# Kernel tuning notes

Measured on AMD Instinct MI355X. Metric: run time of the kernel, lower is better.

The kernel has to match this reference:

```python
import jax, jax.numpy as jnp
import numpy as np

N, V = 256, 5
D_DX, D_RX = 48, 48
C = 128            # code_dim
DEMO_F, DEMO_D = 32, 64
DT, NH, DFF = 256, 8, 2048
REP, HID = 128, 256
NE, NC = 2, 64
VOC_DX = (1000, 5000, 20000)
VOC_RX = (100, 500, 2000, 5000)
NEG = -1e20

def _ln(x, s, b):
    m = jnp.mean(x, -1, keepdims=True)
    v = jnp.var(x, -1, keepdims=True)
    return (x - m) / jnp.sqrt(v + 1e-5) * s + b

def _pe(seq, d):
    pos = jnp.arange(seq, dtype=jnp.float32)[:, None]
    i = jnp.arange(0, d, 2, dtype=jnp.float32)
    ang = pos / jnp.power(10000.0, i / d)
    pe = jnp.zeros((seq, d), jnp.float32)
    pe = pe.at[:, 0::2].set(jnp.sin(ang))
    pe = pe.at[:, 1::2].set(jnp.cos(ang))
    return pe

def _mha(x, qw, qb, ow_, ob_):
    n, s, d = x.shape
    hd = d // NH
    q, k, v = jnp.split(x @ qw + qb, 3, axis=-1)
    q = q.reshape(n, s, NH, hd); k = k.reshape(n, s, NH, hd); v = v.reshape(n, s, NH, hd)
    att = jax.nn.softmax(jnp.einsum('bqhd,bkhd->bhqk', q, k) / jnp.sqrt(jnp.float32(hd)), axis=-1)
    return jnp.einsum('bhqk,bkhd->bqhd', att, v).reshape(n, s, d) @ ow_ + ob_

def _enc_layer(x, qw, qb, ow_, ob_, l1s, l1b, f1w, f1b, f2w, f2b, l2s, l2b):
    x = _ln(x + _mha(x, qw, qb, ow_, ob_), l1s, l1b)            # post-norm, as nn.TransformerEncoderLayer default
    ff = jnp.maximum(x @ f1w + f1b, 0.0) @ f2w + f2b
    return _ln(x + ff, l2s, l2b)

def setup_inputs() -> dict:
    key = jax.random.key(0)
    ks = iter(jax.random.split(key, 96))
    def nrm(shape, scale=0.02):
        return jax.random.normal(next(ks), shape, jnp.float32) * scale
    def zeros(shape): return jnp.zeros(shape, jnp.float32)
    def ones(shape): return jnp.ones(shape, jnp.float32)
    inp = {}
    inp['x_dx_l1'] = jax.random.randint(next(ks), (N, V, D_DX), 0, VOC_DX[0])
    inp['x_dx_l2'] = jax.random.randint(next(ks), (N, V, D_DX), 0, VOC_DX[1])
    inp['x_dx_l3'] = jax.random.randint(next(ks), (N, V, D_DX), 0, VOC_DX[2])
    inp['x_rx_l1'] = jax.random.randint(next(ks), (N, V, D_RX), 0, VOC_RX[0])
    inp['x_rx_l2'] = jax.random.randint(next(ks), (N, V, D_RX), 0, VOC_RX[1])
    inp['x_rx_l3'] = jax.random.randint(next(ks), (N, V, D_RX), 0, VOC_RX[2])
    inp['x_rx_l4'] = jax.random.randint(next(ks), (N, V, D_RX), 0, VOC_RX[3])
    inp['x_demo'] = jax.random.normal(next(ks), (N, V, DEMO_F), jnp.float32)
    inp['W_demo'] = nrm((DEMO_F, DEMO_D)); inp['b_demo'] = zeros((DEMO_D,))
    inp['E_dx1'] = nrm((VOC_DX[0], C)); inp['E_dx2'] = nrm((VOC_DX[1], C)); inp['E_dx3'] = nrm((VOC_DX[2], C))
    inp['E_rx1'] = nrm((VOC_RX[0], C)); inp['E_rx2'] = nrm((VOC_RX[1], C))
    inp['E_rx3'] = nrm((VOC_RX[2], C)); inp['E_rx4'] = nrm((VOC_RX[3], C))
    inp['We_dx'] = nrm((2 * C, 1)); inp['be_dx'] = zeros((1,))
    inp['We_rx'] = nrm((2 * C, 1)); inp['be_rx'] = zeros((1,))
    inp['Wev_dx'] = nrm((C, 1)); inp['bev_dx'] = zeros((1,))
    inp['Wev_rx'] = nrm((C, 1)); inp['bev_rx'] = zeros((1,))
    inp['Wcv'] = nrm((REP, 1)); inp['bcv'] = zeros((1,))
    inp['enc_w1'] = nrm((DEMO_D + C, DT)); inp['enc_b1'] = zeros((DT,))
    inp['qkv_w'] = nrm((4, DT, 3 * DT)); inp['qkv_b'] = zeros((4, 3 * DT))
    inp['ow'] = nrm((4, DT, DT)); inp['ob'] = zeros((4, DT))
    inp['ln1s'] = ones((4, DT)); inp['ln1b'] = zeros((4, DT))
    inp['ff1w'] = nrm((4, DT, DFF)); inp['ff1b'] = zeros((4, DFF))
    inp['ff2w'] = nrm((4, DFF, DT)); inp['ff2b'] = zeros((4, DT))
    inp['ln2s'] = ones((4, DT)); inp['ln2b'] = zeros((4, DT))
    inp['enc_w2'] = nrm((DT, REP)); inp['enc_b2'] = zeros((REP,))
    inp['mlp_w'] = nrm((REP, REP // 2)); inp['mlp_b'] = zeros((REP // 2,))
    inp['mlp2_w'] = nrm((REP // 2, REP // 2)); inp['mlp2_b'] = zeros((REP // 2,))
    inp['fc1w'] = nrm((NE, REP, HID)); inp['fc1b'] = zeros((NE, HID))
    inp['fc2w'] = nrm((NE, HID, HID // 2)); inp['fc2b'] = zeros((NE, HID // 2))
    inp['fc3w'] = nrm((NE, HID // 2, NC)); inp['fc3b'] = zeros((NE, NC))
    return inp

def reference(x_dx_l1, x_dx_l2, x_dx_l3, x_rx_l1, x_rx_l2, x_rx_l3, x_rx_l4, x_demo,
              W_demo, b_demo, E_dx1, E_dx2, E_dx3, E_rx1, E_rx2, E_rx3, E_rx4,
              We_dx, be_dx, We_rx, be_rx, Wev_dx, bev_dx, Wev_rx, bev_rx, Wcv, bcv,
              enc_w1, enc_b1, qkv_w, qkv_b, ow, ob, ln1s, ln1b, ff1w, ff1b, ff2w, ff2b,
              ln2s, ln2b, enc_w2, enc_b2, mlp_w, mlp_b, mlp2_w, mlp2_b,
              fc1w, fc1b, fc2w, fc2b, fc3w, fc3b):
    # ---- GRAM context vectors (dropout is identity at inference) ----
    emb_dx = jnp.stack([E_dx1[x_dx_l1], E_dx2[x_dx_l2], E_dx3[x_dx_l3]], axis=-2)          # [N,V,D,3,C]
    cat_dx = jnp.concatenate([jnp.broadcast_to(emb_dx[..., 2:3, :], emb_dx.shape), emb_dx], axis=-1)
    en_dx = jnp.maximum(cat_dx @ We_dx + be_dx, 0.0)                                       # [N,V,D,3,1]
    en_dx = jnp.where((x_dx_l1 != 0)[..., None, None], en_dx, NEG)
    att_dx = jax.nn.softmax(en_dx, axis=-2)
    cv_dx = jnp.einsum('nvdr,nvdrc->nvdc', att_dx[..., 0], emb_dx)                          # [N,V,D,C]

    emb_rx = jnp.stack([E_rx1[x_rx_l1], E_rx2[x_rx_l2], E_rx3[x_rx_l3], E_rx4[x_rx_l4]], axis=-2)  # [N,V,D,4,C]
    cat_rx = jnp.concatenate([jnp.broadcast_to(emb_rx[..., 3:4, :], emb_rx.shape), emb_rx], axis=-1)
    en_rx = jnp.maximum(cat_rx @ We_rx + be_rx, 0.0)
    en_rx = jnp.where((x_rx_l1 != 0)[..., None, None], en_rx, NEG)
    att_rx = jax.nn.softmax(en_rx, axis=-2)
    cv_rx = jnp.einsum('nvdr,nvdrc->nvdc', att_rx[..., 0], emb_rx)

    # ---- visit-level attention pooling over concatenated codes ----
    context = jnp.concatenate([cv_dx, cv_rx], axis=-2)                                      # [N,V,Ddx+Drx,C]
    ev_dx = jnp.where((x_dx_l1 != 0)[..., None], cv_dx @ Wev_dx + bev_dx, NEG)
    ev_rx = jnp.where((x_rx_l1 != 0)[..., None], cv_rx @ Wev_rx + bev_rx, NEG)
    att_v = jax.nn.softmax(jnp.concatenate([ev_dx, ev_rx], axis=-2), axis=-2)               # [N,V,M,1]
    ccv = jnp.einsum('nvm,nvmc->nvc', att_v[..., 0], context)                               # [N,V,C]

    # ---- shared transformer encoder ----
    demo = jnp.maximum(x_demo @ W_demo + b_demo, 0.0)
    x = jnp.concatenate([demo, ccv], axis=-1) @ enc_w1 + enc_b1
    x = x + _pe(V, DT)[None]
    for i in range(4):
        x = _enc_layer(x, qkv_w[i], qkv_b[i], ow[i], ob[i], ln1s[i], ln1b[i],
                       ff1w[i], ff1b[i], ff2w[i], ff2b[i], ln2s[i], ln2b[i])
    enc = x @ enc_w2 + enc_b2                                                               # [N,V,REP]

    # ---- visit compression ----
    a = jax.nn.softmax(enc @ Wcv + bcv, axis=-2)                                            # [N,V,1]
    civ = jnp.einsum('nv,nvc->nc', a[..., 0], enc)                                          # [N,REP]

    ph = jnp.maximum(civ @ mlp_w + mlp_b, 0.0) @ mlp2_w + mlp2_b                            # [N,REP/2]

    # ---- per-event FC heads (vectorized over events) ----
    h = jnp.maximum(jnp.einsum('nc,ech->neh', civ, fc1w) + fc1b, 0.0)
    h = jnp.maximum(jnp.einsum('neh,ehk->nek', h, fc2w) + fc2b, 0.0)
    out = jax.nn.sigmoid(jnp.einsum('nek,ekm->nem', h, fc3w) + fc3b)                        # [N,NE,NC]
    return out, civ, ph
```

## Files before the change

### kernel.cpp

```cpp
#include <hip/hip_runtime.h>
#include <hip/hip_bf16.h>
#include <math.h>

#define N_PAT 256
#define VIS   5
#define NV    (N_PAT*VIS)
#define DD    48
#define CD    128
#define DT    256
#define HD    32
#define DFF   2048
#define REP   128

#define GF_BIAS 1
#define GF_RELU 2
#define GF_PE   4

typedef __attribute__((ext_vector_type(8))) short short8v;
typedef __attribute__((ext_vector_type(4))) float f32x4;

__device__ __forceinline__ unsigned short f2b(float f) {
    unsigned u = __float_as_uint(f);
    return (unsigned short)((u + 0x7fffu + ((u >> 16) & 1u)) >> 16);
}

__global__ __launch_bounds__(256) void prep_kernel(
    const float* __restrict__ Ed1, const float* __restrict__ Ed2, const float* __restrict__ Ed3,
    const float* __restrict__ Er1, const float* __restrict__ Er2, const float* __restrict__ Er3,
    const float* __restrict__ Er4,
    const float* __restrict__ We_dx, const float* __restrict__ We_rx,
    const float* __restrict__ Wev_dx, const float* __restrict__ Wev_rx,
    float* __restrict__ pe,
    float* __restrict__ pd1, float* __restrict__ pd2, float* __restrict__ pd3,
    float* __restrict__ pr1, float* __restrict__ pr2, float* __restrict__ pr3,
    float* __restrict__ pr4)
{
    const int b = blockIdx.x;
    if (b < VIS) {
        int c = threadIdx.x, j = c >> 1;
        float ang = (float)b / powf(10000.f, (2.f * (float)j) / 256.f);
        pe[b * DT + c] = (c & 1) ? cosf(ang) : sinf(ang);
        return;
    }
    const int g = (b - VIS) * 4 + (threadIdx.x >> 6);
    const int lane = threadIdx.x & 63;
    if (g >= 33600) return;
    const float* E; float* out; int loc; int isdx;
    if      (g < 1000)  { E = Ed1; out = pd1; loc = g;          isdx = 1; }
    else if (g < 6000)  { E = Ed2; out = pd2; loc = g - 1000;   isdx = 1; }
    else if (g < 26000) { E = Ed3; out = pd3; loc = g - 6000;   isdx = 1; }
    else if (g < 26100) { E = Er1; out = pr1; loc = g - 26000;  isdx = 0; }
    else if (g < 26600) { E = Er2; out = pr2; loc = g - 26100;  isdx = 0; }
    else if (g < 28600) { E = Er3; out = pr3; loc = g - 26600;  isdx = 0; }
    else                { E = Er4; out = pr4; loc = g - 28600;  isdx = 0; }
    const float* Wlo = isdx ? We_dx : We_rx;
    const float* Whi = Wlo + CD;
    const float* Wev = isdx ? Wev_dx : Wev_rx;
    float2 e   = *(const float2*)(E + (size_t)loc * CD + lane * 2);
    float2 whi = *(const float2*)(Whi + lane * 2);
    float2 wlo = *(const float2*)(Wlo + lane * 2);
    float2 wev = *(const float2*)(Wev + lane * 2);
    float ph = e.x * whi.x + e.y * whi.y;
    float pl = e.x * wlo.x + e.y * wlo.y;
    float pw = e.x * wev.x + e.y * wev.y;
    #pragma unroll
    for (int off = 32; off; off >>= 1) {
        ph += __shfl_xor(ph, off, 64);
        pl += __shfl_xor(pl, off, 64);
        pw += __shfl_xor(pw, off, 64);
    }
    if (lane == 0) {
        out[(size_t)loc * 4 + 0] = ph;
        out[(size_t)loc * 4 + 1] = pl;
        out[(size_t)loc * 4 + 2] = pw;
        out[(size_t)loc * 4 + 3] = 0.f;
    }
}

__global__ __launch_bounds__(256) void wconv_all(
    const float* __restrict__ qkv_w, unsigned short* __restrict__ qkv_wt,
    const float* __restrict__ ff1w,  unsigned short* __restrict__ ff1_wt,
    const float* __restrict__ ff2w,  unsigned short* __restrict__ ff2_wt,
    const float* __restrict__ ew1,   unsigned short* __restrict__ ew1_t)
{
    __shared__ float t[32][33];
    int b = blockIdx.x;
    const float* src; unsigned short* dst; int K, N, ky, nx;
    if (b < 768) {
        int mat = b / 192, r = b % 192; ky = r / 24; nx = r % 24;
        K = 256; N = 768;
        src = qkv_w + (size_t)mat * K * N; dst = qkv_wt + (size_t)mat * N * K;
    } else if (b < 2816) {
        b -= 768; int mat = b / 512, r = b % 512; ky = r / 64; nx = r % 64;
        K = 256; N = 2048;
        src = ff1w + (size_t)mat * K * N; dst = ff1_wt + (size_t)mat * N * K;
    } else if (b < 4864) {
        b -= 2816; int mat = b / 512, r = b % 512; ky = r / 8; nx = r % 8;
        K = 2048; N = 256;
        src = ff2w + (size_t)mat * K * N; dst = ff2_wt + (size_t)mat * N * K;
    } else {
        b -= 4864; ky = b / 8; nx = b % 8;
        K = 192; N = 256;
        src = ew1; dst = ew1_t;
    }
    int k0 = ky * 32, n0 = nx * 32;
    int tx = threadIdx.x & 31, ty = threadIdx.x >> 5;
    #pragma unroll
    for (int r = ty; r < 32; r += 8) t[r][tx] = src[(size_t)(k0 + r) * N + n0 + tx];
    __syncthreads();
    #pragma unroll
    for (int r = ty; r < 32; r += 8) dst[(size_t)(n0 + r) * K + k0 + tx] = f2b(t[tx][r]);
}

__global__ __launch_bounds__(256) void gram_kernel(
    const int* __restrict__ xd1, const int* __restrict__ xd2, const int* __restrict__ xd3,
    const int* __restrict__ xr1, const int* __restrict__ xr2, const int* __restrict__ xr3,
    const int* __restrict__ xr4,
    const float* __restrict__ Ed1, const float* __restrict__ Ed2, const float* __restrict__ Ed3,
    const float* __restrict__ Er1, const float* __restrict__ Er2, const float* __restrict__ Er3,
    const float* __restrict__ Er4,
    const float* __restrict__ pd1, const float* __restrict__ pd2, const float* __restrict__ pd3,
    const float* __restrict__ pr1, const float* __restrict__ pr2, const float* __restrict__ pr3,
    const float* __restrict__ pr4,
    const float* __restrict__ be_dx, const float* __restrict__ be_rx,
    const float* __restrict__ bev_dx, const float* __restrict__ bev_rx,
    const float* __restrict__ x_demo, const float* __restrict__ W_demo,
    const float* __restrict__ b_demo,
    unsigned short* __restrict__ A0bf)
{
    __shared__ float aw[96][4];
    __shared__ float ev[96];
    __shared__ int   sidx[96][4];
    __shared__ float part[4][128];
    const int nv   = blockIdx.x;
    const int tid  = threadIdx.x;
    const int wave = tid >> 6, lane = tid & 63;
    const int base = nv * DD;

    if (tid < 48) {
        const int d = tid;
        const int i1 = xd1[base + d], i2 = xd2[base + d], i3 = xd3[base + d];
        sidx[d][0] = i1; sidx[d][1] = i2; sidx[d][2] = i3;
        float4 q1 = *(const float4*)(pd1 + (size_t)i1 * 4);
        float4 q2 = *(const float4*)(pd2 + (size_t)i2 * 4);
        float4 q3 = *(const float4*)(pd3 + (size_t)i3 * 4);
        const float be = be_dx[0];
        const float p0 = q3.y;
        float s1 = fmaxf(p0 + q1.x + be, 0.f);
        float s2 = fmaxf(p0 + q2.x + be, 0.f);
        float s3 = fmaxf(p0 + q3.x + be, 0.f);
        float a1, a2, a3;
        if (i1 != 0) {
            float mx = fmaxf(s1, fmaxf(s2, s3));
            a1 = expf(s1 - mx); a2 = expf(s2 - mx); a3 = expf(s3 - mx);
        } else {
            a1 = a2 = a3 = 1.f;
        }
        float inv = 1.f / (a1 + a2 + a3);
        a1 *= inv; a2 *= inv; a3 *= inv;
        aw[d][0] = a1; aw[d][1] = a2; aw[d][2] = a3; aw[d][3] = 0.f;
        ev[d] = (i1 != 0) ? (a1 * q1.z + a2 * q2.z + a3 * q3.z + bev_dx[0]) : -1e20f;
    } else if (tid >= 64 && tid < 112) {
        const int d = tid - 64;
        const int i1 = xr1[base + d], i2 = xr2[base + d], i3 = xr3[base + d], i4 = xr4[base + d];
        const int m = 48 + d;
        sidx[m][0] = i1; sidx[m][1] = i2; sidx[m][2] = i3; sidx[m][3] = i4;
        float4 q1 = *(const float4*)(pr1 + (size_t)i1 * 4);
        float4 q2 = *(const float4*)(pr2 + (size_t)i2 * 4);
        float4 q3 = *(const float4*)(pr3 + (size_t)i3 * 4);
        float4 q4 = *(const float4*)(pr4 + (size_t)i4 * 4);
        const float be = be_rx[0];
        const float p0 = q4.y;
        float s1 = fmaxf(p0 + q1.x + be, 0.f);
        float s2 = fmaxf(p0 + q2.x + be, 0.f);
        float s3 = fmaxf(p0 + q3.x + be, 0.f);
        float s4 = fmaxf(p0 + q4.x + be, 0.f);
        float a1, a2, a3, a4;
        if (i1 != 0) {
            float mx = fmaxf(fmaxf(s1, s2), fmaxf(s3, s4));
            a1 = expf(s1 - mx); a2 = expf(s2 - mx); a3 = expf(s3 - mx); a4 = expf(s4 - mx);
        } else {
            a1 = a2 = a3 = a4 = 1.f;
        }
        float inv = 1.f / (a1 + a2 + a3 + a4);
        aw[m][0] = a1 * inv; aw[m][1] = a2 * inv; aw[m][2] = a3 * inv; aw[m][3] = a4 * inv;
        ev[m] = (i1 != 0) ? ((a1 * q1.z + a2 * q2.z + a3 * q3.z + a4 * q4.z) * inv + bev_rx[0])
                          : -1e20f;
    }
    __syncthreads();

    if (wave == 0) {
        float a = ev[lane];
        float b = (lane < 32) ? ev[64 + lane] : -3.0e38f;
        float mx = fmaxf(a, b);
        #pragma unroll
        for (int off = 32; off; off >>= 1) mx = fmaxf(mx, __shfl_xor(mx, off, 64));
        float ea = expf(a - mx);
        float eb = (lane < 32) ? expf(b - mx) : 0.f;
        float s = ea + eb;
        #pragma unroll
        for (int off = 32; off; off >>= 1) s += __shfl_xor(s, off, 64);
        float inv = 1.f / s;
        ev[lane] = ea * inv;
        if (lane < 32) ev[64 + lane] = eb * inv;
    }
    __syncthreads();

    if (tid < 96) {
        float av = ev[tid];
        aw[tid][0] *= av; aw[tid][1] *= av; aw[tid][2] *= av; aw[tid][3] *= av;
    }
    __syncthreads();

    float accx = 0.f, accy = 0.f;
    const int co = lane * 2;
    for (int m = wave; m < 96; m += 4) {
        if (m < 48) {
            int i1 = sidx[m][0], i2 = sidx[m][1], i3 = sidx[m][2];
            float2 e1 = *(const float2*)(Ed1 + (size_t)i1 * CD + co);
            float2 e2 = *(const float2*)(Ed2 + (size_t)i2 * CD + co);
            float2 e3 = *(const float2*)(Ed3 + (size_t)i3 * CD + co);
            float w1 = aw[m][0], w2 = aw[m][1], w3 = aw[m][2];
            accx += w1 * e1.x + w2 * e2.x + w3 * e3.x;
            accy += w1 * e1.y + w2 * e2.y + w3 * e3.y;
        } else {
            int i1 = sidx[m][0], i2 = sidx[m][1], i3 = sidx[m][2], i4 = sidx[m][3];
            float2 e1 = *(const float2*)(Er1 + (size_t)i1 * CD + co);
            float2 e2 = *(const float2*)(Er2 + (size_t)i2 * CD + co);
            float2 e3 = *(const float2*)(Er3 + (size_t)i3 * CD + co);
            float2 e4 = *(const float2*)(Er4 + (size_t)i4 * CD + co);
            float w1 = aw[m][0], w2 = aw[m][1], w3 = aw[m][2], w4 = aw[m][3];
            accx += w1 * e1.x + w2 * e2.x + w3 * e3.x + w4 * e4.x;
            accy += w1 * e1.y + w2 * e2.y + w3 * e3.y + w4 * e4.y;
        }
    }
    part[wave][co]     = accx;
    part[wave][co + 1] = accy;
    __syncthreads();
    if (tid < CD) {
        A0bf[(size_t)nv * 192 + 64 + tid] =
            f2b(part[0][tid] + part[1][tid] + part[2][tid] + part[3][tid]);
    } else if (tid >= 192) {
        int j = tid - 192;
        float acc = b_demo[j];
        #pragma unroll
        for (int f = 0; f < 32; ++f) acc += x_demo[nv * 32 + f] * W_demo[f * 64 + j];
        A0bf[(size_t)nv * 192 + j] = f2b(fmaxf(acc, 0.f));
    }
}

__global__ __launch_bounds__(256) void gemm_bf(
    const unsigned short* __restrict__ A, const unsigned short* __restrict__ B,
    const float* __restrict__ bias, const float* __restrict__ pe,
    float* __restrict__ Cf, unsigned short* __restrict__ Cb,
    int M, int N, int K, int flags, int kchunk)
{
    __shared__ unsigned short As[64][40];
    __shared__ unsigned short Bs[64][40];
    const int bm = blockIdx.y * 64, bn = blockIdx.x * 64;
    const int tid = threadIdx.x;
    const int wave = tid >> 6, lane = tid & 63;
    const int wr = (wave >> 1) * 32, wc = (wave & 1) * 32;
    const int l15 = lane & 15, l4 = lane >> 4;
    const int srow = tid >> 2, sk8 = (tid & 3) * 8;
    const int kbeg = blockIdx.z * kchunk, kend = kbeg + kchunk;
    f32x4 acc[2][2] = {};

    for (int k0 = kbeg; k0 < kend; k0 += 32) {
        *(short8v*)&As[srow][sk8] = *(const short8v*)(A + (size_t)(bm + srow) * K + k0 + sk8);
        *(short8v*)&Bs[srow][sk8] = *(const short8v*)(B + (size_t)(bn + srow) * K + k0 + sk8);
        __syncthreads();
        short8v a0 = *(const short8v*)&As[wr + l15][l4 * 8];
        short8v a1 = *(const short8v*)&As[wr + 16 + l15][l4 * 8];
        short8v b0 = *(const short8v*)&Bs[wc + l15][l4 * 8];
        short8v b1 = *(const short8v*)&Bs[wc + 16 + l15][l4 * 8];
        acc[0][0] = __builtin_amdgcn_mfma_f32_16x16x32_bf16(a0, b0, acc[0][0], 0, 0, 0);
        acc[0][1] = __builtin_amdgcn_mfma_f32_16x16x32_bf16(a0, b1, acc[0][1], 0, 0, 0);
        acc[1][0] = __builtin_amdgcn_mfma_f32_16x16x32_bf16(a1, b0, acc[1][0], 0, 0, 0);
        acc[1][1] = __builtin_amdgcn_mfma_f32_16x16x32_bf16(a1, b1, acc[1][1], 0, 0, 0);
        __syncthreads();
    }

    if (gridDim.z == 1) {
        #pragma unroll
        for (int mi = 0; mi < 2; ++mi)
            #pragma unroll
            for (int ni = 0; ni < 2; ++ni) {
                int col = bn + wc + ni * 16 + l15;
                float bz = (flags & GF_BIAS) ? bias[col] : 0.f;
                #pragma unroll
                for (int r = 0; r < 4; ++r) {
                    int row = bm + wr + mi * 16 + l4 * 4 + r;
                    float v = acc[mi][ni][r] + bz;
                    if (flags & GF_PE)   v += pe[(row % VIS) * N + col];
                    if (flags & GF_RELU) v = fmaxf(v, 0.f);
                    if (Cf) Cf[(size_t)row * N + col] = v;
                    if (Cb) Cb[(size_t)row * N + col] = f2b(v);
                }
            }
    } else {
        float* Cp = Cf + (size_t)blockIdx.z * M * N;
        #pragma unroll
        for (int mi = 0; mi < 2; ++mi)
            #pragma unroll
            for (int ni = 0; ni < 2; ++ni) {
                int col = bn + wc + ni * 16 + l15;
                #pragma unroll
                for (int r = 0; r < 4; ++r) {
                    int row = bm + wr + mi * 16 + l4 * 4 + r;
                    Cp[(size_t)row * N + col] = acc[mi][ni][r];
                }
            }
    }
}

__global__ __launch_bounds__(256) void gemm_k(
    const float* __restrict__ A, const float* __restrict__ B,
    float* __restrict__ C, int M, int N, int K, int kchunk)
{
    __shared__ float As[16][68];
    __shared__ float Bs[16][64];
    const int bm = blockIdx.y * 64, bn = blockIdx.x * 64;
    const int tid = threadIdx.x;
    const int tx = tid & 15, ty = tid >> 4;
    const int kbeg = blockIdx.z * kchunk;
    const int kend = kbeg + kchunk;
    const int ar  = tid >> 2, akc = (tid & 3) * 4;
    const int bbr = tid >> 4, bbc = (tid & 15) * 4;
    float acc[4][4] = {{0.f}};

    for (int k0 = kbeg; k0 < kend; k0 += 16) {
        float4 va = *(const float4*)(A + (size_t)(bm + ar) * K + k0 + akc);
        float4 vb = *(const float4*)(B + (size_t)(k0 + bbr) * N + bn + bbc);
        As[akc + 0][ar] = va.x;
        As[akc + 1][ar] = va.y;
        As[akc + 2][ar] = va.z;
        As[akc + 3][ar] = va.w;
        *(float4*)&Bs[bbr][bbc] = vb;
        __syncthreads();
        #pragma unroll
        for (int kk = 0; kk < 16; ++kk) {
            float4 a = *(const float4*)&As[kk][ty * 4];
            float4 b = *(const float4*)&Bs[kk][tx * 4];
            acc[0][0] += a.x * b.x; acc[0][1] += a.x * b.y; acc[0][2] += a.x * b.z; acc[0][3] += a.x * b.w;
            acc[1][0] += a.y * b.x; acc[1][1] += a.y * b.y; acc[1][2] += a.y * b.z; acc[1][3] += a.y * b.w;
            acc[2][0] += a.z * b.x; acc[2][1] += a.z * b.y; acc[2][2] += a.z * b.z; acc[2][3] += a.z * b.w;
            acc[3][0] += a.w * b.x; acc[3][1] += a.w * b.y; acc[3][2] += a.w * b.z; acc[3][3] += a.w * b.w;
        }
        __syncthreads();
    }

    float* Cp = C + (size_t)blockIdx.z * M * N;
    #pragma unroll
    for (int i = 0; i < 4; ++i) {
        int row = bm + ty * 4 + i;
        *(float4*)(Cp + (size_t)row * N + bn + tx * 4) = *(float4*)&acc[i][0];
    }
}

__global__ void reduce_kernel(
    const float* __restrict__ part, int S, int MN,
    const float* __restrict__ bias,
    const float* __restrict__ resid,
    const float* __restrict__ lns, const float* __restrict__ lnb,
    int N, float* __restrict__ out, unsigned short* __restrict__ out_bf)
{
    const int row = blockIdx.x, t = threadIdx.x;
    const size_t idx = (size_t)row * N + t;
    float v = bias[t];
    for (int s = 0; s < S; ++s) v += part[(size_t)s * MN + idx];
    if (resid) v += resid[idx];
    if (lns) {
        float s1 = v, s2 = v * v;
        #pragma unroll
        for (int off = 32; off; off >>= 1) {
            s1 += __shfl_xor(s1, off, 64);
            s2 += __shfl_xor(s2, off, 64);
        }
        __shared__ float red[2][4];
        const int wave = t >> 6, lane = t & 63, nw = blockDim.x >> 6;
        if (lane == 0) { red[0][wave] = s1; red[1][wave] = s2; }
        __syncthreads();
        s1 = 0.f; s2 = 0.f;
        for (int w = 0; w < nw; ++w) { s1 += red[0][w]; s2 += red[1][w]; }
        float invn = 1.f / (float)N;
        float m    = s1 * invn;
        float var  = s2 * invn - m * m;
        float inv  = 1.f / sqrtf(var + 1e-5f);
        v = (v - m) * inv * lns[t] + lnb[t];
    }
    out[idx] = v;
    if (out_bf) out_bf[idx] = f2b(v);
}

__global__ __launch_bounds__(256) void attn_proj_ln(
    const float* __restrict__ qkv,
    const float* __restrict__ ow,
    const float* __restrict__ ob,
    const float* __restrict__ lns, const float* __restrict__ lnb,
    float* __restrict__ xbuf, unsigned short* __restrict__ xbuf_bf)
{
    __shared__ float attn_s[VIS][DT];
    __shared__ float red[VIS][2][4];
    const int n = blockIdx.x;
    const int tid = threadIdx.x;
    const int h = tid >> 5, t = tid & 31;
    const int ch = h * HD + t;

    {
        float q[VIS], k[VIS], v[VIS];
        #pragma unroll
        for (int j = 0; j < VIS; ++j) {
            const float* row = qkv + (size_t)(n * VIS + j) * 768 + ch;
            q[j] = row[0]; k[j] = row[256]; v[j] = row[512];
        }
        const float scale = 0.1767766952966369f;
        float sm[VIS][VIS];
        #pragma unroll
        for (int qi = 0; qi < VIS; ++qi)
            #pragma unroll
            for (int ki = 0; ki < VIS; ++ki) {
                float p = q[qi] * k[ki];
                #pragma unroll
                for (int off = 16; off; off >>= 1) p += __shfl_xor(p, off, 32);
                sm[qi][ki] = p * scale;
            }
        #pragma unroll
        for (int qi = 0; qi < VIS; ++qi) {
            float mx = sm[qi][0];
            #pragma unroll
            for (int ki = 1; ki < VIS; ++ki) mx = fmaxf(mx, sm[qi][ki]);
            float e[VIS], sum = 0.f;
            #pragma unroll
            for (int ki = 0; ki < VIS; ++ki) { e[ki] = expf(sm[qi][ki] - mx); sum += e[ki]; }
            float inv = 1.f / sum;
            float acc = 0.f;
            #pragma unroll
            for (int ki = 0; ki < VIS; ++ki) acc += e[ki] * inv * v[ki];
            attn_s[qi][ch] = acc;
        }
    }
    __syncthreads();

    const int c = tid;
    float acc[VIS] = {0.f, 0.f, 0.f, 0.f, 0.f};
    #pragma unroll 4
    for (int k = 0; k < DT; ++k) {
        float w = ow[(size_t)k * DT + c];
        #pragma unroll
        for (int j = 0; j < VIS; ++j) acc[j] += attn_s[j][k] * w;
    }
    float bz = ob[c];
    float v[VIS];
    #pragma unroll
    for (int j = 0; j < VIS; ++j)
        v[j] = acc[j] + bz + xbuf[(size_t)(n * VIS + j) * DT + c];

    const int wave = tid >> 6, lane = tid & 63;
    #pragma unroll
    for (int j = 0; j < VIS; ++j) {
        float s1 = v[j], s2 = v[j] * v[j];
        #pragma unroll
        for (int off = 32; off; off >>= 1) {
            s1 += __shfl_xor(s1, off, 64);
            s2 += __shfl_xor(s2, off, 64);
        }
        if (lane == 0) { red[j][0][wave] = s1; red[j][1][wave] = s2; }
    }
    __syncthreads();
    #pragma unroll
    for (int j = 0; j < VIS; ++j) {
        float s1 = red[j][0][0] + red[j][0][1] + red[j][0][2] + red[j][0][3];
        float s2 = red[j][1][0] + red[j][1][1] + red[j][1][2] + red[j][1][3];
        float m   = s1 * (1.f / 256.f);
        float var = s2 * (1.f / 256.f) - m * m;
        float inv = 1.f / sqrtf(var + 1e-5f);
        float o = (v[j] - m) * inv * lns[c] + lnb[c];
        size_t idx = (size_t)(n * VIS + j) * DT + c;
        xbuf[idx] = o;
        xbuf_bf[idx] = f2b(o);
    }
}

__global__ __launch_bounds__(128) void vc_ph_kernel(
    const float* __restrict__ encp, int S, int MN, const float* __restrict__ enc_b2,
    const float* __restrict__ Wcv, const float* __restrict__ bcv,
    const float* __restrict__ mlp_w, const float* __restrict__ mlp_b,
    const float* __restrict__ mlp2_w, const float* __restrict__ mlp2_b,
    float* __restrict__ civ_out, float* __restrict__ ph_out)
{
    const int n = blockIdx.x, t = threadIdx.x;
    const int wave = t >> 6, lane = t & 63;
    float e[VIS];
    #pragma unroll
    for (int v = 0; v < VIS; ++v) {
        size_t idx = (size_t)(n * VIS + v) * REP + t;
        float ev = enc_b2[t];
        for (int s = 0; s < S; ++s) ev += encp[(size_t)s * MN + idx];
        e[v] = ev;
    }
    float w = Wcv[t];
    __shared__ float part[VIS][2];
    #pragma unroll
    for (int v = 0; v < VIS; ++v) {
        float pv = e[v] * w;
        #pragma unroll
        for (int off = 32; off; off >>= 1) pv += __shfl_xor(pv, off, 64);
        if (lane == 0) part[v][wave] = pv;
    }
    __syncthreads();
    float b0 = bcv[0];
    float sc[VIS], mx = -3e38f;
    #pragma unroll
    for (int v = 0; v < VIS; ++v) { sc[v] = part[v][0] + part[v][1] + b0; mx = fmaxf(mx, sc[v]); }
    float sum = 0.f;
    #pragma unroll
    for (int v = 0; v < VIS; ++v) { sc[v] = expf(sc[v] - mx); sum += sc[v]; }
    float inv = 1.f / sum;
    float civ = 0.f;
    #pragma unroll
    for (int v = 0; v < VIS; ++v) civ += sc[v] * inv * e[v];
    civ_out[(size_t)n * REP + t] = civ;

    __shared__ float civ_s[REP];
    __shared__ float h1_s[64];
    civ_s[t] = civ;
    __syncthreads();
    if (t < 64) {
        float acc = mlp_b[t];
        #pragma unroll 8
        for (int c = 0; c < REP; ++c) acc += civ_s[c] * mlp_w[c * 64 + t];
        h1_s[t] = fmaxf(acc, 0.f);
    }
    __syncthreads();
    if (t < 64) {
        float acc = mlp2_b[t];
        #pragma unroll 8
        for (int j = 0; j < 64; ++j) acc += h1_s[j] * mlp2_w[j * 64 + t];
        ph_out[(size_t)n * 64 + t] = acc;
    }
}

__global__ __launch_bounds__(256) void heads_kernel(
    const float* __restrict__ civ,
    const float* __restrict__ fc1w, const float* __restrict__ fc1b,
    const float* __restrict__ fc2w, const float* __restrict__ fc2b,
    const float* __restrict__ fc3w, const float* __restrict__ fc3b,
    float* __restrict__ out)
{
    const int n = blockIdx.x >> 1, e = blockIdx.x & 1;
    const int t = threadIdx.x;
    __shared__ float civ_s[REP], h1[256], h2[128];
    if (t < REP) civ_s[t] = civ[(size_t)n * REP + t];
    __syncthreads();
    {
        float acc = fc1b[e * 256 + t];
        const float* w = fc1w + (size_t)e * REP * 256;
        #pragma unroll 8
        for (int c = 0; c < REP; ++c) acc += civ_s[c] * w[c * 256 + t];
        h1[t] = fmaxf(acc, 0.f);
    }
    __syncthreads();
    if (t < 128) {
        float acc = fc2b[e * 128 + t];
        const float* w = fc2w + (size_t)e * 256 * 128;
        #pragma unroll 8
        for (int c = 0; c < 256; ++c) acc += h1[c] * w[c * 128 + t];
        h2[t] = fmaxf(acc, 0.f);
    }
    __syncthreads();
    if (t < 64) {
        float acc = fc3b[e * 64 + t];
        const float* w = fc3w + (size_t)e * 128 * 64;
        #pragma unroll 8
        for (int c = 0; c < 128; ++c) acc += h2[c] * w[c * 64 + t];
        out[(size_t)(n * 2 + e) * 64 + t] = 1.f / (1.f + expf(-acc));
    }
}

extern "C" void kernel_launch(void* const* d_in, const int* in_sizes, int n_in,
                              void* d_out, int out_size, void* d_ws, size_t ws_size,
                              hipStream_t stream) {
    const int*   xd1    = (const int*)  d_in[0];
    const int*   xd2    = (const int*)  d_in[1];
    const int*   xd3    = (const int*)  d_in[2];
    const int*   xr1    = (const int*)  d_in[3];
    const int*   xr2    = (const int*)  d_in[4];
    const int*   xr3    = (const int*)  d_in[5];
    const int*   xr4    = (const int*)  d_in[6];
    const float* x_demo = (const float*)d_in[7];
    const float* W_demo = (const float*)d_in[8];
    const float* b_demo = (const float*)d_in[9];
    const float* Ed1    = (const float*)d_in[10];
    const float* Ed2    = (const float*)d_in[11];
    const float* Ed3    = (const float*)d_in[12];
    const float* Er1    = (const float*)d_in[13];
    const float* Er2    = (const float*)d_in[14];
    const float* Er3    = (const float*)d_in[15];
    const float* Er4    = (const float*)d_in[16];
    const float* We_dx  = (const float*)d_in[17];
    const float* be_dx  = (const float*)d_in[18];
    const float* We_rx  = (const float*)d_in[19];
    const float* be_rx  = (const float*)d_in[20];
    const float* Wev_dx = (const float*)d_in[21];
    const float* bev_dx = (const float*)d_in[22];
    const float* Wev_rx = (const float*)d_in[23];
    const float* bev_rx = (const float*)d_in[24];
    const float* Wcv    = (const float*)d_in[25];
    const float* bcv    = (const float*)d_in[26];
    const float* enc_w1 = (const float*)d_in[27];
    const float* enc_b1 = (const float*)d_in[28];
    const float* qkv_w  = (const float*)d_in[29];
    const float* qkv_b  = (const float*)d_in[30];
    const float* ow     = (const float*)d_in[31];
    const float* ob     = (const float*)d_in[32];
    const float* ln1s   = (const float*)d_in[33];
    const float* ln1b   = (const float*)d_in[34];
    const float* ff1w   = (const float*)d_in[35];
    const float* ff1b   = (const float*)d_in[36];
    const float* ff2w   = (const float*)d_in[37];
    const float* ff2b   = (const float*)d_in[38];
    const float* ln2s   = (const float*)d_in[39];
    const float* ln2b   = (const float*)d_in[40];
    const float* enc_w2 = (const float*)d_in[41];
    const float* enc_b2 = (const float*)d_in[42];
    const float* mlp_w  = (const float*)d_in[43];
    const float* mlp_b  = (const float*)d_in[44];
    const float* mlp2_w = (const float*)d_in[45];
    const float* mlp2_b = (const float*)d_in[46];
    const float* fc1w   = (const float*)d_in[47];
    const float* fc1b   = (const float*)d_in[48];
    const float* fc2w   = (const float*)d_in[49];
    const float* fc2b   = (const float*)d_in[50];
    const float* fc3w   = (const float*)d_in[51];
    const float* fc3b   = (const float*)d_in[52];

    float* ws     = (float*)d_ws;
    float* pe     = ws;
    float* xbuf   = pe + 1280;
    float* qkvbuf = xbuf + 327680;
    float* buf2   = qkvbuf + 983040;
    float* ptab   = buf2 + 1310720;
    unsigned short* usb = (unsigned short*)(ptab + 134400);
    unsigned short* A0bf    = usb;
    unsigned short* xbuf_bf = A0bf + 245760;
    unsigned short* ff1_bf  = xbuf_bf + 327680;
    unsigned short* qkv_wt  = ff1_bf + 2621440;
    unsigned short* ff1_wt  = qkv_wt + 786432;
    unsigned short* ff2_wt  = ff1_wt + 2097152;
    unsigned short* ew1_t   = ff2_wt + 2097152;

    float* pd1 = ptab;
    float* pd2 = pd1 + 4000;
    float* pd3 = pd2 + 20000;
    float* pr1 = pd3 + 80000;
    float* pr2 = pr1 + 400;
    float* pr3 = pr2 + 2000;
    float* pr4 = pr3 + 8000;

    prep_kernel<<<5 + 8400, 256, 0, stream>>>(Ed1, Ed2, Ed3, Er1, Er2, Er3, Er4,
                                              We_dx, We_rx, Wev_dx, Wev_rx,
                                              pe, pd1, pd2, pd3, pr1, pr2, pr3, pr4);
    wconv_all<<<4912, 256, 0, stream>>>(qkv_w, qkv_wt, ff1w, ff1_wt, ff2w, ff2_wt,
                                        enc_w1, ew1_t);
    gram_kernel<<<NV, 256, 0, stream>>>(xd1, xd2, xd3, xr1, xr2, xr3, xr4,
                                        Ed1, Ed2, Ed3, Er1, Er2, Er3, Er4,
                                        pd1, pd2, pd3, pr1, pr2, pr3, pr4,
                                        be_dx, be_rx, bev_dx, bev_rx,
                                        x_demo, W_demo, b_demo, A0bf);

    gemm_bf<<<dim3(4, 20, 1), 256, 0, stream>>>(A0bf, ew1_t, enc_b1, pe,
                                                xbuf, xbuf_bf, NV, DT, 192,
                                                GF_BIAS | GF_PE, 192);

    for (int i = 0; i < 4; ++i) {
        gemm_bf<<<dim3(12, 20, 1), 256, 0, stream>>>(
            xbuf_bf, qkv_wt + (size_t)i * 768 * 256, qkv_b + i * 768, nullptr,
            qkvbuf, nullptr, NV, 768, DT, GF_BIAS, DT);
        attn_proj_ln<<<N_PAT, 256, 0, stream>>>(
            qkvbuf, ow + (size_t)i * DT * DT, ob + i * DT,
            ln1s + i * DT, ln1b + i * DT, xbuf, xbuf_bf);
        gemm_bf<<<dim3(32, 20, 1), 256, 0, stream>>>(
            xbuf_bf, ff1_wt + (size_t)i * DFF * 256, ff1b + i * DFF, nullptr,
            nullptr, ff1_bf, NV, DFF, DT, GF_BIAS | GF_RELU, DT);
        gemm_bf<<<dim3(4, 20, 4), 256, 0, stream>>>(
            ff1_bf, ff2_wt + (size_t)i * 256 * DFF, nullptr, nullptr,
            buf2, nullptr, NV, DT, DFF, 0, 512);
        reduce_kernel<<<NV, DT, 0, stream>>>(buf2, 4, NV * DT, ff2b + i * DT,
                                             xbuf, ln2s + i * DT, ln2b + i * DT,
                                             DT, xbuf, xbuf_bf);
    }

    gemm_k<<<dim3(2, 20, 8), 256, 0, stream>>>(xbuf, enc_w2, buf2, NV, REP, DT, 32);

    float* civ_out = (float*)d_out + 32768;
    float* ph_out  = (float*)d_out + 65536;
    vc_ph_kernel<<<N_PAT, 128, 0, stream>>>(buf2, 8, NV * REP, enc_b2,
                                            Wcv, bcv, mlp_w, mlp_b, mlp2_w, mlp2_b,
                                            civ_out, ph_out);
    heads_kernel<<<N_PAT * 2, 256, 0, stream>>>(civ_out, fc1w, fc1b, fc2w, fc2b, fc3w, fc3b,
                                                (float*)d_out);
}
```

Baseline: 480.4 us.

## Double GEMM K-step to 64 and add split-K for QKV and FF2

The bf16 GEMM now stages 64-wide K slices in shared memory per iteration and issues two MFMA rounds per tile, halving the number of barrier pairs per K. The QKV projection becomes split-K over two slices, with the partial sums and bias folded into the attention kernel's loads. FF2 split-K goes from 4 to 8 slices, and the workspace is enlarged to hold the partials. This adds more partial-sum traffic and a larger shared-memory footprint in exchange for more blocks in flight and fewer synchronisations.

```diff
diff --git a/kernel.cpp b/kernel.cpp
--- a/kernel.cpp
+++ b/kernel.cpp
@@ -255,8 +255,8 @@
     float* __restrict__ Cf, unsigned short* __restrict__ Cb,
     int M, int N, int K, int flags, int kchunk)
 {
-    __shared__ unsigned short As[64][40];
-    __shared__ unsigned short Bs[64][40];
+    __shared__ unsigned short As[64][72];
+    __shared__ unsigned short Bs[64][72];
     const int bm = blockIdx.y * 64, bn = blockIdx.x * 64;
     const int tid = threadIdx.x;
     const int wave = tid >> 6, lane = tid & 63;
@@ -266,18 +266,25 @@
     const int kbeg = blockIdx.z * kchunk, kend = kbeg + kchunk;
     f32x4 acc[2][2] = {};
 
-    for (int k0 = kbeg; k0 < kend; k0 += 32) {
-        *(short8v*)&As[srow][sk8] = *(const short8v*)(A + (size_t)(bm + srow) * K + k0 + sk8);
-        *(short8v*)&Bs[srow][sk8] = *(const short8v*)(B + (size_t)(bn + srow) * K + k0 + sk8);
+    for (int k0 = kbeg; k0 < kend; k0 += 64) {
+        const unsigned short* Ap = A + (size_t)(bm + srow) * K + k0 + sk8;
+        const unsigned short* Bp = B + (size_t)(bn + srow) * K + k0 + sk8;
+        *(short8v*)&As[srow][sk8]      = *(const short8v*)(Ap);
+        *(short8v*)&As[srow][sk8 + 32] = *(const short8v*)(Ap + 32);
+        *(short8v*)&Bs[srow][sk8]      = *(const short8v*)(Bp);
+        *(short8v*)&Bs[srow][sk8 + 32] = *(const short8v*)(Bp + 32);
         __syncthreads();
-        short8v a0 = *(const short8v*)&As[wr + l15][l4 * 8];
-        short8v a1 = *(const short8v*)&As[wr + 16 + l15][l4 * 8];
-        short8v b0 = *(const short8v*)&Bs[wc + l15][l4 * 8];
-        short8v b1 = *(const short8v*)&Bs[wc + 16 + l15][l4 * 8];
-        acc[0][0] = __builtin_amdgcn_mfma_f32_16x16x32_bf16(a0, b0, acc[0][0], 0, 0, 0);
-        acc[0][1] = __builtin_amdgcn_mfma_f32_16x16x32_bf16(a0, b1, acc[0][1], 0, 0, 0);
-        acc[1][0] = __builtin_amdgcn_mfma_f32_16x16x32_bf16(a1, b0, acc[1][0], 0, 0, 0);
-        acc[1][1] = __builtin_amdgcn_mfma_f32_16x16x32_bf16(a1, b1, acc[1][1], 0, 0, 0);
+        #pragma unroll
+        for (int h = 0; h < 2; ++h) {
+            short8v a0 = *(const short8v*)&As[wr + l15][h * 32 + l4 * 8];
+            short8v a1 = *(const short8v*)&As[wr + 16 + l15][h * 32 + l4 * 8];
+            short8v b0 = *(const short8v*)&Bs[wc + l15][h * 32 + l4 * 8];
+            short8v b1 = *(const short8v*)&Bs[wc + 16 + l15][h * 32 + l4 * 8];
+            acc[0][0] = __builtin_amdgcn_mfma_f32_16x16x32_bf16(a0, b0, acc[0][0], 0, 0, 0);
+            acc[0][1] = __builtin_amdgcn_mfma_f32_16x16x32_bf16(a0, b1, acc[0][1], 0, 0, 0);
+            acc[1][0] = __builtin_amdgcn_mfma_f32_16x16x32_bf16(a1, b0, acc[1][0], 0, 0, 0);
+            acc[1][1] = __builtin_amdgcn_mfma_f32_16x16x32_bf16(a1, b1, acc[1][1], 0, 0, 0);
+        }
         __syncthreads();
     }
 
@@ -394,7 +401,8 @@
 }
 
 __global__ __launch_bounds__(256) void attn_proj_ln(
-    const float* __restrict__ qkv,
+    const float* __restrict__ qkvp, int S, int MN,
+    const float* __restrict__ qb,
     const float* __restrict__ ow,
     const float* __restrict__ ob,
     const float* __restrict__ lns, const float* __restrict__ lnb,
@@ -411,8 +419,13 @@
         float q[VIS], k[VIS], v[VIS];
         #pragma unroll
         for (int j = 0; j < VIS; ++j) {
-            const float* row = qkv + (size_t)(n * VIS + j) * 768 + ch;
-            q[j] = row[0]; k[j] = row[256]; v[j] = row[512];
+            size_t idx = (size_t)(n * VIS + j) * 768 + ch;
+            float qq = qb[ch], kk = qb[256 + ch], vv = qb[512 + ch];
+            for (int s = 0; s < S; ++s) {
+                const float* p = qkvp + (size_t)s * MN + idx;
+                qq += p[0]; kk += p[256]; vv += p[512];
+            }
+            q[j] = qq; k[j] = kk; v[j] = vv;
         }
         const float scale = 0.1767766952966369f;
         float sm[VIS][VIS];
@@ -639,8 +652,8 @@
     float* pe     = ws;
     float* xbuf   = pe + 1280;
     float* qkvbuf = xbuf + 327680;
-    float* buf2   = qkvbuf + 983040;
-    float* ptab   = buf2 + 1310720;
+    float* buf2   = qkvbuf + 1966080;
+    float* ptab   = buf2 + 2621440;
     unsigned short* usb = (unsigned short*)(ptab + 134400);
     unsigned short* A0bf    = usb;
     unsigned short* xbuf_bf = A0bf + 245760;
@@ -674,19 +687,20 @@
                                                 GF_BIAS | GF_PE, 192);
 
     for (int i = 0; i < 4; ++i) {
-        gemm_bf<<<dim3(12, 20, 1), 256, 0, stream>>>(
-            xbuf_bf, qkv_wt + (size_t)i * 768 * 256, qkv_b + i * 768, nullptr,
-            qkvbuf, nullptr, NV, 768, DT, GF_BIAS, DT);
+        gemm_bf<<<dim3(12, 20, 2), 256, 0, stream>>>(
+            xbuf_bf, qkv_wt + (size_t)i * 768 * 256, nullptr, nullptr,
+            qkvbuf, nullptr, NV, 768, DT, 0, 128);
         attn_proj_ln<<<N_PAT, 256, 0, stream>>>(
-            qkvbuf, ow + (size_t)i * DT * DT, ob + i * DT,
+            qkvbuf, 2, NV * 768, qkv_b + i * 768,
+            ow + (size_t)i * DT * DT, ob + i * DT,
             ln1s + i * DT, ln1b + i * DT, xbuf, xbuf_bf);
         gemm_bf<<<dim3(32, 20, 1), 256, 0, stream>>>(
             xbuf_bf, ff1_wt + (size_t)i * DFF * 256, ff1b + i * DFF, nullptr,
             nullptr, ff1_bf, NV, DFF, DT, GF_BIAS | GF_RELU, DT);
-        gemm_bf<<<dim3(4, 20, 4), 256, 0, stream>>>(
+        gemm_bf<<<dim3(4, 20, 8), 256, 0, stream>>>(
             ff1_bf, ff2_wt + (size_t)i * 256 * DFF, nullptr, nullptr,
-            buf2, nullptr, NV, DT, DFF, 0, 512);
-        reduce_kernel<<<NV, DT, 0, stream>>>(buf2, 4, NV * DT, ff2b + i * DT,
+            buf2, nullptr, NV, DT, DFF, 0, 256);
+        reduce_kernel<<<NV, DT, 0, stream>>>(buf2, 8, NV * DT, ff2b + i * DT,
                                              xbuf, ln2s + i * DT, ln2b + i * DT,
                                              DT, xbuf, xbuf_bf);
     }
```

New measurement: 492.1 us. +2.4%, slower.
